# Optimization experiments

Hardware: AMD Instinct MI355X
Metric: run time of the kernel (lower is better)

Reference implementation:

```python
import jax, jax.numpy as jnp
import numpy as np

T, H, W, B = 9, 128, 128, 8  # size=[9,128,128], 8 samples in batch
N = 4194304


def _avg3(x):
    # AvgPool3d(kernel=(1,3,3), stride=1, pad=(0,1,1), count_include_pad=True)
    s = jax.lax.reduce_window(x, 0.0, jax.lax.add, (1, 1, 1, 3, 3), (1, 1, 1, 1, 1),
                              ((0, 0), (0, 0), (0, 0), (1, 1), (1, 1)))
    return s / 9.0


def _inorm(x, eps=1e-5):
    # InstanceNorm3d(affine=False): normalize over (T,H,W) per sample/channel
    m = x.mean(axis=(2, 3, 4), keepdims=True)
    v = x.var(axis=(2, 3, 4), keepdims=True)
    return (x - m) * jax.lax.rsqrt(v + eps)


def _time_corr(x):
    bx = (x > 0).astype(x.dtype)
    bx = jnp.concatenate([bx, bx[:, :, -1:]], axis=2)  # ReplicationPad3d back in T
    prev = _avg3(bx)
    around = (prev[:, :, :-1] * bx[:, :, 1:] > 4.0 / 9.0).astype(x.dtype)
    return _avg3(around)


def _dyn_conv(x, fc1_w, fc2_w, dyn_w):
    # Dynamic_Conv, kernel (3,1,1): attention over k=4 weight banks, per-sample conv
    a = x.mean(axis=(2, 3, 4))                       # [B,C] global avg pool
    a = jax.nn.relu(a @ fc1_w.T)
    a = jax.nn.softmax(a @ fc2_w.T, axis=1)          # [B,k]
    w = jnp.einsum('bk,koid->boid', a, dyn_w)        # [B,O,I,3]
    xp = jnp.pad(x, ((0, 0), (0, 0), (1, 1), (0, 0), (0, 0)))  # pad T
    t = x.shape[2]
    out = jnp.einsum('boi,bithw->bothw', w[..., 0], xp[:, :, 0:t])
    out = out + jnp.einsum('boi,bithw->bothw', w[..., 1], xp[:, :, 1:1 + t])
    out = out + jnp.einsum('boi,bithw->bothw', w[..., 2], xp[:, :, 2:2 + t])
    return out


def _voxelize(t, x, y, p, b):
    # per-batch normalize t by max, then bilinear-in-time scatter-add over T bins
    tmax = jax.ops.segment_max(t, b, num_segments=B)
    ts = (t / tmax[b]) * T                                         # [N]
    bins = jnp.arange(T, dtype=ts.dtype)
    vals = jnp.maximum(1.0 - jnp.abs(ts[None, :] - bins[:, None]), 0.0)  # [T,N]
    base = x + W * y + W * H * T * p + 2 * W * H * T * b           # [N]
    idx = base[None, :] + W * H * jnp.arange(T, dtype=base.dtype)[:, None]
    vox = jnp.zeros(B * 2 * T * H * W, dtype=ts.dtype).at[idx].add(vals)
    return vox.reshape(B, 2, T, H, W)


def setup_inputs() -> dict:
    key = jax.random.key(0)
    ks = jax.random.split(key, 10)
    t = jax.random.uniform(ks[0], (N,), dtype=jnp.float32)
    x = jax.random.randint(ks[1], (N,), 0, W, dtype=jnp.int32)
    y = jax.random.randint(ks[2], (N,), 0, H, dtype=jnp.int32)
    p = jax.random.randint(ks[3], (N,), 0, 2, dtype=jnp.int32)
    b = jnp.sort(jax.random.randint(ks[4], (N,), 0, B, dtype=jnp.int32))
    conv1_w = jax.random.normal(ks[5], (16, 2), jnp.float32) / np.sqrt(2.0)
    fc1_w = jax.random.normal(ks[6], (8, 16), jnp.float32) / np.sqrt(16.0)
    fc2_w = jax.random.normal(ks[7], (4, 8), jnp.float32) / np.sqrt(8.0)
    dyn_w = jax.random.normal(ks[8], (4, 16, 16, 3), jnp.float32) / np.sqrt(48.0)
    conv3_w = jax.random.normal(ks[9], (2, 16), jnp.float32) / np.sqrt(16.0)
    return {"t": t, "x": x, "y": y, "p": p, "b": b,
            "conv1_w": conv1_w, "fc1_w": fc1_w, "fc2_w": fc2_w,
            "dyn_w": dyn_w, "conv3_w": conv3_w}


def reference(t, x, y, p, b, conv1_w, fc1_w, fc2_w, dyn_w, conv3_w):
    vox = _voxelize(t, x, y, p, b)                     # [B,2,T,H,W]
    mask = _time_corr(vox)
    h = _inorm(vox)
    h = jnp.einsum('oc,bcthw->bothw', conv1_w, h)      # 1x1x1 conv 2->16
    h = _dyn_conv(h, fc1_w, fc2_w, dyn_w)
    h = jnp.einsum('oc,bcthw->bothw', conv3_w, h)      # 1x1x1 conv 16->2
    out = _inorm(jax.nn.sigmoid(h) * mask)
    return out
```

## Files before the change

### kernel.cpp

```cpp
#include <hip/hip_runtime.h>
#include <math.h>

#define TT 9
#define HH 128
#define WW 128
#define BB 8
#define SLICE (HH*WW)
#define CHW (TT*SLICE)
#define BCH (2*CHW)
#define TOT (BB*BCH)
#define INV_M (1.0f/147456.0f)
#define NYG 16
#define NBK (9*NYG)
#define SEGCAP 8192u
#define SSCALE 274877906944.0f
#define INV_SSCALE (1.0/274877906944.0)

__global__ void __launch_bounds__(1024) k_bounds(
        const int* __restrict__ b, int* __restrict__ start, int n,
        const float* __restrict__ conv1_w, const float* __restrict__ dyn_w,
        const float* __restrict__ conv3_w, float* __restrict__ Kc,
        unsigned* __restrict__ cursor) {
    if (blockIdx.x == 1) {
        for (int i = threadIdx.x; i < 8 * NBK; i += 1024)
            cursor[i] = (unsigned)i * SEGCAP;
        return;
    }
    int tid = threadIdx.x;
    if (tid < 9) {
        if (tid == 0) start[0] = 0;
        else if (tid == 8) start[8] = n;
        else {
            int lo = 0, hi = n;
            while (lo < hi) { int mid = (lo + hi) >> 1; if (b[mid] < tid) lo = mid + 1; else hi = mid; }
            start[tid] = lo;
        }
    }
    if (tid >= 32 && tid < 44) {
        int q = tid - 32;
        int d = q % 3, c = (q / 3) & 1, o2 = q / 6;
        float acc = 0.0f;
        for (int o = 0; o < 16; ++o) {
            float c3 = conv3_w[o2 * 16 + o];
            for (int i = 0; i < 16; ++i) {
                float wsum = 0.0f;
                for (int k = 0; k < 4; ++k) wsum += dyn_w[((k * 16 + o) * 16 + i) * 3 + d];
                acc += c3 * (0.25f * wsum) * conv1_w[i * 2 + c];
            }
        }
        Kc[q] = acc;
    }
}

__global__ void __launch_bounds__(1024) k_tmax(
        const float* __restrict__ t, const int* __restrict__ start,
        unsigned* __restrict__ gmax) {
    __shared__ unsigned sm[1024];
    int bi = blockIdx.x & 7, cj = blockIdx.x >> 3, nb = gridDim.x >> 3;
    int s = start[bi], e = start[bi + 1];
    unsigned m = 0u;
    if (e > s) {
        int a = (s + 3) & ~3; if (a > e) a = e;
        int z = e & ~3;       if (z < a) z = a;
        if (cj == 0) {
            int i = s + (int)threadIdx.x;
            if (i < a) { unsigned v = __float_as_uint(t[i]); if (v > m) m = v; }
            i = z + (int)threadIdx.x;
            if (i < e) { unsigned v = __float_as_uint(t[i]); if (v > m) m = v; }
        }
        long nq = (long)(z - a) >> 2;
        long per = (nq + nb - 1) / nb;
        long q0 = (long)cj * per; if (q0 > nq) q0 = nq;
        long q1 = q0 + per;       if (q1 > nq) q1 = nq;
        const float4* tp = (const float4*)(t + a);
        for (long i = q0 + threadIdx.x; i < q1; i += 1024) {
            float4 u = tp[i];
            unsigned c = __float_as_uint(fmaxf(fmaxf(u.x, u.y), fmaxf(u.z, u.w)));
            if (c > m) m = c;
        }
    }
    sm[threadIdx.x] = m;
    __syncthreads();
    for (int ofs = 512; ofs > 0; ofs >>= 1) {
        if (threadIdx.x < ofs && sm[threadIdx.x + ofs] > sm[threadIdx.x])
            sm[threadIdx.x] = sm[threadIdx.x + ofs];
        __syncthreads();
    }
    if (threadIdx.x == 0 && sm[0]) atomicMax(&gmax[bi], sm[0]);
}

__global__ void __launch_bounds__(1024) k_place(
        const float* __restrict__ t, const int* __restrict__ x,
        const int* __restrict__ y, const int* __restrict__ p,
        const unsigned* __restrict__ gmax, const int* __restrict__ start,
        unsigned* __restrict__ cursor, int2* __restrict__ rec) {
    __shared__ unsigned lh[NBK], lc[NBK];
    int bi = blockIdx.x & 7, cj = blockIdx.x >> 3, nb = gridDim.x >> 3;
    int s = start[bi], e = start[bi + 1];
    if (e <= s) return;
    float tmax = __uint_as_float(gmax[bi]);
    int a = (s + 3) & ~3; if (a > e) a = e;
    int z = e & ~3;       if (z < a) z = a;
    long nq = (long)(z - a) >> 2;
    long per = (nq + nb - 1) / nb;
    long q0 = (long)cj * per; if (q0 > nq) q0 = nq;
    long q1 = q0 + per;       if (q1 > nq) q1 = nq;
    const float4* tp = (const float4*)(t + a);
    const int4*   xp = (const int4*)(x + a);
    const int4*   yp = (const int4*)(y + a);
    const int4*   pp = (const int4*)(p + a);
    for (long base = q0; base < q1; base += 2048) {
        for (int j = threadIdx.x; j < NBK; j += 1024) lh[j] = 0u;
        __syncthreads();
        int lb[8]; float tsv[8]; int keyv[8]; unsigned rank[8];
        #pragma unroll
        for (int h = 0; h < 2; ++h) {
            long qi = base + h * 1024 + threadIdx.x;
            #pragma unroll
            for (int k = 0; k < 4; ++k) lb[h * 4 + k] = -1;
            if (qi < q1) {
                float4 tv = tp[qi]; int4 xv = xp[qi]; int4 yv = yp[qi]; int4 pv = pp[qi];
                float tq[4] = {tv.x, tv.y, tv.z, tv.w};
                int   xq[4] = {xv.x, xv.y, xv.z, xv.w};
                int   yq[4] = {yv.x, yv.y, yv.z, yv.w};
                int   pq[4] = {pv.x, pv.y, pv.z, pv.w};
                #pragma unroll
                for (int k = 0; k < 4; ++k) {
                    float ts = tq[k] / tmax * 9.0f;
                    int i0 = (int)floorf(ts);
                    if ((unsigned)i0 < 9u) {
                        lb[h * 4 + k] = i0 * NYG + (yq[k] >> 3);
                        tsv[h * 4 + k] = ts;
                        keyv[h * 4 + k] = xq[k] + (yq[k] << 7) + (pq[k] << 14);
                    }
                }
            }
        }
        #pragma unroll
        for (int k = 0; k < 8; ++k)
            if (lb[k] >= 0) rank[k] = atomicAdd(&lh[lb[k]], 1u);
        __syncthreads();
        for (int j = threadIdx.x; j < NBK; j += 1024) {
            unsigned c = lh[j];
            lc[j] = c ? atomicAdd(&cursor[bi * NBK + j], c) : 0u;
        }
        __syncthreads();
        #pragma unroll
        for (int k = 0; k < 8; ++k)
            if (lb[k] >= 0) {
                unsigned slot = lc[lb[k]] + rank[k];
                if (slot < (unsigned)(bi * NBK + lb[k] + 1) * SEGCAP)
                    rec[slot] = make_int2(__float_as_int(tsv[k]), keyv[k]);
            }
        __syncthreads();
    }
    if (cj == 0) {
        int i = -1;
        if ((int)threadIdx.x < a - s) i = s + threadIdx.x;
        else if (threadIdx.x >= 64 && (int)(threadIdx.x - 64) < e - z) i = z + (threadIdx.x - 64);
        if (i >= 0) {
            float ts = t[i] / tmax * 9.0f;
            int i0 = (int)floorf(ts);
            if ((unsigned)i0 < 9u) {
                int lbx = i0 * NYG + (y[i] >> 3);
                unsigned slot = atomicAdd(&cursor[bi * NBK + lbx], 1u);
                if (slot < (unsigned)(bi * NBK + lbx + 1) * SEGCAP)
                    rec[slot] = make_int2(__float_as_int(ts), x[i] + (y[i] << 7) + (p[i] << 14));
            }
        }
    }
}

#define CELL(K) (((K) & 1023) | (((K) >> 4) & 1024))
#define DEP1(TSB, KEY) { float ts_ = __int_as_float(TSB); \
    unsigned long long sq_ = (unsigned long long)(ts_ * SSCALE); \
    atomicAdd(&asl[CELL(KEY)], (1ull << 48) | sq_); }

__global__ void __launch_bounds__(1024) k_accum(
        const int2* __restrict__ rec, const unsigned* __restrict__ cursor,
        unsigned long long* __restrict__ Abuf) {
    __shared__ unsigned long long asl[2048];
    int tg = blockIdx.x, bb = blockIdx.y, yg = blockIdx.z;
    asl[threadIdx.x] = 0ull; asl[1024 + threadIdx.x] = 0ull;
    __syncthreads();
    int lb = bb * NBK + tg * NYG + yg;
    unsigned s = (unsigned)lb * SEGCAP;
    unsigned e = cursor[lb];
    unsigned cap = s + SEGCAP; if (e > cap) e = cap;
    unsigned a = (s + 1) & ~1u, z = e & ~1u; if (z < a) z = a;
    if (threadIdx.x == 0 && s < a && s < e) { int2 r = rec[s]; DEP1(r.x, r.y) }
    if (threadIdx.x == 1 && z < e)          { int2 r = rec[z]; DEP1(r.x, r.y) }
    int n2 = (int)((z - a) >> 1);
    const int4* rp = (const int4*)(rec + a);
    for (int i = threadIdx.x; i < n2; i += 1024) {
        int4 q = rp[i];
        DEP1(q.x, q.y)
        DEP1(q.z, q.w)
    }
    __syncthreads();
    unsigned long long* Ao = Abuf + s;
    Ao[threadIdx.x]        = asl[threadIdx.x];
    Ao[1024 + threadIdx.x] = asl[1024 + threadIdx.x];
}

__global__ void __launch_bounds__(256) k_recon(
        const unsigned long long* __restrict__ Abuf,
        float* __restrict__ vox, float* __restrict__ s1) {
    int idx = blockIdx.x * 256 + threadIdx.x;
    int cell = idx & 2047;
    int yg = (idx >> 11) & 15;
    int bb = idx >> 15;
    unsigned long long Av[9];
    #pragma unroll
    for (int t = 0; t < 9; ++t)
        Av[t] = Abuf[(size_t)(unsigned)(bb * NBK + t * NYG + yg) * SEGCAP + cell];
    int p = cell >> 10, row = (cell >> 7) & 7, xx = cell & 127;
    float* vp = vox + (size_t)bb * BCH + (size_t)p * CHW + (size_t)(((yg << 3) + row) << 7) + xx;
    double Cp = 0.0, Sp = 0.0;
    float ls = 0.f, lq = 0.f;
    #pragma unroll
    for (int t = 0; t < 9; ++t) {
        double C = (double)(unsigned)(Av[t] >> 48);
        double S = (double)(Av[t] & 0xFFFFFFFFFFFFull) * INV_SSCALE;
        float v = (float)(C * (double)(1 + t) - S + (Sp - Cp * (double)(t - 1)));
        vp[t * SLICE] = v;
        ls += v; lq += v * v;
        Cp = C; Sp = S;
    }
    __shared__ float ss[256], sq[256];
    ss[threadIdx.x] = ls; sq[threadIdx.x] = lq;
    __syncthreads();
    for (int ofs = 128; ofs > 0; ofs >>= 1) {
        if (threadIdx.x < ofs) { ss[threadIdx.x] += ss[threadIdx.x + ofs]; sq[threadIdx.x] += sq[threadIdx.x + ofs]; }
        __syncthreads();
    }
    if (threadIdx.x == 0) {
        int bc = bb * 2 + p;
        atomicAdd(&s1[bc], ss[0]); atomicAdd(&s1[16 + bc], sq[0]);
    }
}

__global__ void __launch_bounds__(1024, 4) k_scat(
        const float* __restrict__ t, const int* __restrict__ x,
        const int* __restrict__ y, const int* __restrict__ p,
        const unsigned* __restrict__ gmax, const int* __restrict__ start,
        float* __restrict__ vox) {
    __shared__ float sl[2 * SLICE];
    int tg = blockIdx.x, bb = blockIdx.y;
    int cs = start[bb], ce = start[bb + 1];
    for (int j = threadIdx.x; j < 2 * SLICE; j += 1024) sl[j] = 0.0f;
    __syncthreads();
    float tmax = __uint_as_float(gmax[bb]);
    float ftg = (float)tg;
    for (int i = cs + threadIdx.x; i < ce; i += 1024) {
        float ts = t[i] / tmax * 9.0f;
        float fl = floorf(ts);
        int i0 = (int)fl;
        bool h0 = (i0 == tg), h1 = (i0 + 1 == tg);
        if (h0 | h1) {
            float w = h0 ? (1.0f - (ts - fl)) : (1.0f - (ftg - ts));
            int hw = x[i] + (y[i] << 7) + (p[i] << 14);
            atomicAdd(&sl[hw], w);
        }
    }
    __syncthreads();
    float* dst = vox + (size_t)bb * BCH + (size_t)tg * SLICE;
    for (int j = threadIdx.x; j < SLICE; j += 1024) {
        dst[j]       = sl[j];
        dst[CHW + j] = sl[SLICE + j];
    }
}

__global__ void k_stats1(const float* __restrict__ vox, float* __restrict__ s1) {
    __shared__ float ss[256], sq[256];
    int bc = blockIdx.x >> 5, part = blockIdx.x & 31;
    const float4* vp = (const float4*)(vox + (long)bc * CHW);
    const int per = (CHW / 4) / 32;
    float s = 0.f, q = 0.f;
    for (int j = part * per + threadIdx.x; j < (part + 1) * per; j += 256) {
        float4 v = vp[j];
        s += v.x + v.y + v.z + v.w;
        q += v.x * v.x + v.y * v.y + v.z * v.z + v.w * v.w;
    }
    ss[threadIdx.x] = s; sq[threadIdx.x] = q;
    __syncthreads();
    for (int ofs = 128; ofs > 0; ofs >>= 1) {
        if (threadIdx.x < ofs) { ss[threadIdx.x] += ss[threadIdx.x + ofs]; sq[threadIdx.x] += sq[threadIdx.x + ofs]; }
        __syncthreads();
    }
    if (threadIdx.x == 0) { atomicAdd(&s1[bc], ss[0]); atomicAdd(&s1[16 + bc], sq[0]); }
}

#define STRIP 32
__global__ void k_mask(const float* __restrict__ vox, float* __restrict__ mask) {
    __shared__ unsigned char sbx[36 * 128];
    __shared__ unsigned char sar[34 * 128];
    int bid = blockIdx.x;
    int strip = bid & 3;
    int t = (bid >> 2) % 9;
    int c = (bid / 36) & 1;
    int bb = bid / 72;
    long off = (long)bb * BCH + (long)c * CHW;
    const float* vt = vox + off + (long)t * SLICE;
    int tn = (t + 1 < 9) ? t + 1 : 8;
    const float* vn = vox + off + (long)tn * SLICE;
    int y0 = strip * STRIP;
    for (int j = threadIdx.x; j < 36 * 128; j += 256) {
        int r = j >> 7, xx = j & 127;
        int gy = y0 - 2 + r;
        sbx[j] = ((unsigned)gy < 128u && vt[(gy << 7) + xx] > 0.0f) ? 1 : 0;
    }
    __syncthreads();
    for (int j = threadIdx.x; j < 34 * 128; j += 256) {
        int ra = j >> 7, xx = j & 127;
        int gy = y0 - 1 + ra;
        unsigned char v = 0;
        if ((unsigned)gy < 128u) {
            int s = 0;
            for (int rs = ra; rs <= ra + 2; ++rs)
                for (int dx = -1; dx <= 1; ++dx) {
                    int x2 = xx + dx; if ((unsigned)x2 >= 128u) continue;
                    s += sbx[(rs << 7) + x2];
                }
            v = (vn[(gy << 7) + xx] > 0.0f && s >= 5) ? 1 : 0;
        }
        sar[j] = v;
    }
    __syncthreads();
    float* mt = mask + off + (long)t * SLICE;
    for (int j = threadIdx.x; j < STRIP * 128; j += 256) {
        int q = j >> 7, xx = j & 127;
        int s = 0;
        for (int ra = q; ra <= q + 2; ++ra)
            for (int dx = -1; dx <= 1; ++dx) {
                int x2 = xx + dx; if ((unsigned)x2 >= 128u) continue;
                s += sar[(ra << 7) + x2];
            }
        mt[((y0 + q) << 7) + xx] = (float)s / 9.0f;
    }
}

__global__ void __launch_bounds__(256) k_g(
        const float* __restrict__ vox, float* __restrict__ gm,
        const float* __restrict__ s1, const float* __restrict__ Kc,
        float* __restrict__ s2) {
    __shared__ float snrm[32];
    if (threadIdx.x < 16) {
        float mm = s1[threadIdx.x] * INV_M;
        float var = s1[16 + threadIdx.x] * INV_M - mm * mm;
        float inv = rsqrtf(var + 1e-5f);
        snrm[threadIdx.x] = inv;
        snrm[16 + threadIdx.x] = -mm * inv;
    }
    __syncthreads();
    int idx = blockIdx.x * 256 + threadIdx.x;
    int hw = idx & (SLICE - 1);
    int o2 = (idx >> 14) & 1;
    int bb = idx >> 15;
    const float* v0 = vox + (size_t)bb * BCH + hw;
    const float* v1 = v0 + CHW;
    float* go = gm + (size_t)bb * BCH + (size_t)o2 * CHW + hw;
    float a[9], d[9], m[9];
    #pragma unroll
    for (int tt = 0; tt < 9; ++tt) a[tt] = v0[tt * SLICE];
    #pragma unroll
    for (int tt = 0; tt < 9; ++tt) d[tt] = v1[tt * SLICE];
    #pragma unroll
    for (int tt = 0; tt < 9; ++tt) m[tt] = go[tt * SLICE];
    float sc0 = snrm[bb * 2], sh0 = snrm[16 + bb * 2];
    float sc1 = snrm[bb * 2 + 1], sh1 = snrm[16 + bb * 2 + 1];
    float k00 = Kc[o2 * 6 + 0], k01 = Kc[o2 * 6 + 1], k02 = Kc[o2 * 6 + 2];
    float k10 = Kc[o2 * 6 + 3], k11 = Kc[o2 * 6 + 4], k12 = Kc[o2 * 6 + 5];
    #pragma unroll
    for (int tt = 0; tt < 9; ++tt) { a[tt] = a[tt] * sc0 + sh0; d[tt] = d[tt] * sc1 + sh1; }
    float ls = 0.f, lq = 0.f;
    #pragma unroll
    for (int tt = 0; tt < 9; ++tt) {
        float pre = k01 * a[tt] + k11 * d[tt];
        if (tt > 0) pre += k00 * a[tt - 1] + k10 * d[tt - 1];
        if (tt < 8) pre += k02 * a[tt + 1] + k12 * d[tt + 1];
        float sig = 1.0f / (1.0f + expf(-pre));
        float g = sig * m[tt];
        go[tt * SLICE] = g;
        ls += g; lq += g * g;
    }
    __shared__ float ss[256], sq[256];
    ss[threadIdx.x] = ls; sq[threadIdx.x] = lq;
    __syncthreads();
    for (int ofs = 128; ofs > 0; ofs >>= 1) {
        if (threadIdx.x < ofs) { ss[threadIdx.x] += ss[threadIdx.x + ofs]; sq[threadIdx.x] += sq[threadIdx.x + ofs]; }
        __syncthreads();
    }
    if (threadIdx.x == 0) {
        int bc = bb * 2 + o2;
        atomicAdd(&s2[bc], ss[0]); atomicAdd(&s2[16 + bc], sq[0]);
    }
}

__global__ void k_norm(float* __restrict__ out, const float* __restrict__ s2) {
    int i4 = blockIdx.x * 256 + threadIdx.x;
    int bc = i4 / (CHW / 4);
    float m = s2[bc] * INV_M;
    float var = s2[16 + bc] * INV_M - m * m;
    float inv = rsqrtf(var + 1e-5f);
    float4 v = ((float4*)out)[i4];
    v.x = (v.x - m) * inv; v.y = (v.y - m) * inv;
    v.z = (v.z - m) * inv; v.w = (v.w - m) * inv;
    ((float4*)out)[i4] = v;
}

extern "C" void kernel_launch(void* const* d_in, const int* in_sizes, int n_in,
                              void* d_out, int out_size, void* d_ws, size_t ws_size,
                              hipStream_t stream) {
    const float* t  = (const float*)d_in[0];
    const int*   x  = (const int*)d_in[1];
    const int*   y  = (const int*)d_in[2];
    const int*   p  = (const int*)d_in[3];
    const int*   b  = (const int*)d_in[4];
    const float* conv1_w = (const float*)d_in[5];
    const float* dyn_w   = (const float*)d_in[8];
    const float* conv3_w = (const float*)d_in[9];
    float* out = (float*)d_out;
    int n = in_sizes[0];

    const long RECF = 2L * 8 * NBK * SEGCAP;
    long availF = (long)(ws_size / sizeof(float));
    long need = (long)TOT + RECF + 4096;
    int useBuckets = (availF >= need);

    float* ws   = (float*)d_ws;
    float* vox  = ws;
    int2*  rec  = (int2*)(ws + TOT);
    float* tail = ws + TOT + (useBuckets ? RECF : 0);
    unsigned* gmax    = (unsigned*)tail;
    float*    s1      = tail + 8;
    float*    s2      = tail + 40;
    float*    Kc      = tail + 72;
    int*      start   = (int*)(tail + 84);
    unsigned* cursor  = (unsigned*)(tail + 96);

    hipMemsetAsync(tail, 0, 72 * sizeof(float), stream);

    k_bounds<<<2, 1024, 0, stream>>>(b, start, n, conv1_w, dyn_w, conv3_w, Kc, cursor);
    k_tmax<<<256, 1024, 0, stream>>>(t, start, gmax);
    if (useBuckets) {
        k_place<<<512, 1024, 0, stream>>>(t, x, y, p, gmax, start, cursor, rec);
        k_accum<<<dim3(9, 8, NYG), 1024, 0, stream>>>(rec, cursor,
                                                      (unsigned long long*)rec);
        k_recon<<<1024, 256, 0, stream>>>((const unsigned long long*)rec, vox, s1);
    } else {
        k_scat<<<dim3(9, 8, 1), 1024, 0, stream>>>(t, x, y, p, gmax, start, vox);
        k_stats1<<<512, 256, 0, stream>>>(vox, s1);
    }
    k_mask<<<576, 256, 0, stream>>>(vox, out);
    k_g<<<1024, 256, 0, stream>>>(vox, out, s1, Kc, s2);
    k_norm<<<TOT / 1024, 256, 0, stream>>>(out, s2);
}
```

Baseline: 153.9 us.

## Stage bucketed event records in shared memory for coalesced global writes

```diff
diff --git a/kernel.cpp b/kernel.cpp
--- a/kernel.cpp
+++ b/kernel.cpp
@@ -94,7 +94,10 @@
         const int* __restrict__ y, const int* __restrict__ p,
         const unsigned* __restrict__ gmax, const int* __restrict__ start,
         unsigned* __restrict__ cursor, int2* __restrict__ rec) {
-    __shared__ unsigned lh[NBK], lc[NBK];
+    __shared__ unsigned lh[NBK], lc[NBK], cbase[NBK];
+    __shared__ unsigned wsum[3];
+    __shared__ int2 srec[4096];
+    __shared__ unsigned char sbkt[4096];
     int bi = blockIdx.x & 7, cj = blockIdx.x >> 3, nb = gridDim.x >> 3;
     int s = start[bi], e = start[bi + 1];
     if (e <= s) return;
@@ -109,49 +112,74 @@
     const int4*   xp = (const int4*)(x + a);
     const int4*   yp = (const int4*)(y + a);
     const int4*   pp = (const int4*)(p + a);
-    for (long base = q0; base < q1; base += 2048) {
-        for (int j = threadIdx.x; j < NBK; j += 1024) lh[j] = 0u;
-        __syncthreads();
-        int lb[8]; float tsv[8]; int keyv[8]; unsigned rank[8];
+    for (long base = q0; base < q1; base += 1024) {
+        if (threadIdx.x < NBK) lh[threadIdx.x] = 0u;
+        __syncthreads();
+        long qi = base + threadIdx.x;
+        int lb[4]; float tsv[4]; int keyv[4]; unsigned rank[4];
         #pragma unroll
-        for (int h = 0; h < 2; ++h) {
-            long qi = base + h * 1024 + threadIdx.x;
+        for (int k = 0; k < 4; ++k) lb[k] = -1;
+        if (qi < q1) {
+            float4 tv = tp[qi]; int4 xv = xp[qi]; int4 yv = yp[qi]; int4 pv = pp[qi];
+            float tq[4] = {tv.x, tv.y, tv.z, tv.w};
+            int   xq[4] = {xv.x, xv.y, xv.z, xv.w};
+            int   yq[4] = {yv.x, yv.y, yv.z, yv.w};
+            int   pq[4] = {pv.x, pv.y, pv.z, pv.w};
             #pragma unroll
-            for (int k = 0; k < 4; ++k) lb[h * 4 + k] = -1;
-            if (qi < q1) {
-                float4 tv = tp[qi]; int4 xv = xp[qi]; int4 yv = yp[qi]; int4 pv = pp[qi];
-                float tq[4] = {tv.x, tv.y, tv.z, tv.w};
-                int   xq[4] = {xv.x, xv.y, xv.z, xv.w};
-                int   yq[4] = {yv.x, yv.y, yv.z, yv.w};
-                int   pq[4] = {pv.x, pv.y, pv.z, pv.w};
-                #pragma unroll
-                for (int k = 0; k < 4; ++k) {
-                    float ts = tq[k] / tmax * 9.0f;
-                    int i0 = (int)floorf(ts);
-                    if ((unsigned)i0 < 9u) {
-                        lb[h * 4 + k] = i0 * NYG + (yq[k] >> 3);
-                        tsv[h * 4 + k] = ts;
-                        keyv[h * 4 + k] = xq[k] + (yq[k] << 7) + (pq[k] << 14);
-                    }
+            for (int k = 0; k < 4; ++k) {
+                float ts = tq[k] / tmax * 9.0f;
+                int i0 = (int)floorf(ts);
+                if ((unsigned)i0 < 9u) {
+                    lb[k] = i0 * NYG + (yq[k] >> 3);
+                    tsv[k] = ts;
+                    keyv[k] = xq[k] + (yq[k] << 7) + (pq[k] << 14);
                 }
             }
         }
         #pragma unroll
-        for (int k = 0; k < 8; ++k)
+        for (int k = 0; k < 4; ++k)
             if (lb[k] >= 0) rank[k] = atomicAdd(&lh[lb[k]], 1u);
         __syncthreads();
-        for (int j = threadIdx.x; j < NBK; j += 1024) {
-            unsigned c = lh[j];
-            lc[j] = c ? atomicAdd(&cursor[bi * NBK + j], c) : 0u;
+        unsigned v = 0, inc = 0;
+        if (threadIdx.x < 192) {
+            v = (threadIdx.x < NBK) ? lh[threadIdx.x] : 0u;
+            inc = v;
+            #pragma unroll
+            for (int ofs = 1; ofs < 64; ofs <<= 1) {
+                unsigned u = __shfl_up(inc, ofs, 64);
+                if ((threadIdx.x & 63) >= ofs) inc += u;
+            }
+            if ((threadIdx.x & 63) == 63) wsum[threadIdx.x >> 6] = inc;
+        }
+        __syncthreads();
+        if (threadIdx.x < NBK) {
+            unsigned ex = inc - v;
+            int w = threadIdx.x >> 6;
+            if (w >= 1) ex += wsum[0];
+            if (w >= 2) ex += wsum[1];
+            cbase[threadIdx.x] = ex;
+            lc[threadIdx.x] = v ? atomicAdd(&cursor[bi * NBK + threadIdx.x], v) : 0u;
         }
         __syncthreads();
         #pragma unroll
-        for (int k = 0; k < 8; ++k)
+        for (int k = 0; k < 4; ++k)
             if (lb[k] >= 0) {
-                unsigned slot = lc[lb[k]] + rank[k];
-                if (slot < (unsigned)(bi * NBK + lb[k] + 1) * SEGCAP)
-                    rec[slot] = make_int2(__float_as_int(tsv[k]), keyv[k]);
-            }
+                unsigned sl_ = cbase[lb[k]] + rank[k];
+                srec[sl_] = make_int2(__float_as_int(tsv[k]), keyv[k]);
+                sbkt[sl_] = (unsigned char)lb[k];
+            }
+        __syncthreads();
+        unsigned tot = cbase[NBK - 1] + lh[NBK - 1];
+        #pragma unroll
+        for (int h = 0; h < 4; ++h) {
+            unsigned slot = threadIdx.x + h * 1024;
+            if (slot < tot) {
+                int bkt = sbkt[slot];
+                unsigned dst = lc[bkt] + (slot - cbase[bkt]);
+                if (dst < (unsigned)(bi * NBK + bkt + 1) * SEGCAP)
+                    rec[dst] = srec[slot];
+            }
+        }
         __syncthreads();
     }
     if (cj == 0) {
```

Measured after the change: 139.8 us. 1.1x faster.
